# Performance work log

Hardware: AMD Instinct MI355X
Metric: run time of the kernel (lower is better)

## Reference

```python
import jax, jax.numpy as jnp
import numpy as np

BN_EPS = 1e-5  # torch BatchNorm1d default


def setup_inputs() -> dict:
    key = jax.random.key(0)
    k = jax.random.split(key, 5)
    B, D, L = 4096, 4096, 4  # batch, width, num layers (3 hidden + 1 output)
    x = jax.random.normal(k[0], (B, D), dtype=jnp.float32)
    # Per-layer Linear weights stored as [L, in, out]; scaled like xavier-ish init.
    W = jax.random.normal(k[1], (L, D, D), dtype=jnp.float32) * (1.0 / np.sqrt(D))
    b = jax.random.normal(k[2], (L, D), dtype=jnp.float32) * 0.01
    gamma = jax.random.uniform(k[3], (L, D), dtype=jnp.float32, minval=0.5, maxval=1.5)
    beta = jax.random.normal(k[4], (L, D), dtype=jnp.float32) * 0.1
    return {"x": x, "W": W, "b": b, "gamma": gamma, "beta": beta}


def _layer(h, W_l, b_l, gamma_l, beta_l):
    # one big GEMM replaces the per-neuron GEMV loop + stack
    h = h @ W_l + b_l  # [B, out]
    # BatchNorm1d, training mode: biased batch stats over the batch dim
    mu = jnp.mean(h, axis=0)
    var = jnp.var(h, axis=0)
    h = (h - mu) * jax.lax.rsqrt(var + BN_EPS) * gamma_l + beta_l
    return jax.nn.relu(h)


def reference(x, W, b, gamma, beta):
    out = x
    for l in range(W.shape[0]):  # small fixed layer count
        out = _layer(out, W[l], b[l], gamma[l], beta[l])
    # nn.Softmax(dim=0): softmax over the batch dimension, as in the original
    return jax.nn.softmax(out, axis=0)
```

## Files before the change

### kernel.cpp

```cpp
#include <hip/hip_runtime.h>
#include <stdint.h>

#define DIMD 4096
#define DIMB 4096
#define NLAYER 4
#define NT (DIMD / 64)

typedef unsigned short u16;
typedef __attribute__((ext_vector_type(4))) float f32x4;
typedef __attribute__((ext_vector_type(8))) __bf16 bf16x8;

__device__ __forceinline__ u16 f2bf(float f) {
    union { float f; uint32_t u; } v; v.f = f;
    return (u16)((v.u + 0x7fffu + ((v.u >> 16) & 1u)) >> 16);
}

__global__ void k_cvt(const float* __restrict__ in, u16* __restrict__ out) {
    int i = (blockIdx.x * 256 + threadIdx.x) * 4;
    float4 v = *reinterpret_cast<const float4*>(in + i);
    ushort4 r;
    r.x = f2bf(v.x); r.y = f2bf(v.y); r.z = f2bf(v.z); r.w = f2bf(v.w);
    *reinterpret_cast<ushort4*>(out + i) = r;
}

__global__ void k_trans(const float* __restrict__ W, u16* __restrict__ Wt) {
    __shared__ float tile[64][65];
    const int t = threadIdx.x;
    const size_t loff = (size_t)blockIdx.z * DIMD * DIMD;
    const int n0 = blockIdx.x * 64, k0 = blockIdx.y * 64;
    const int kr = t >> 4, c4 = (t & 15) * 4;
    #pragma unroll
    for (int r = 0; r < 4; ++r) {
        float4 v = *reinterpret_cast<const float4*>(W + loff + (size_t)(k0 + kr + r * 16) * DIMD + n0 + c4);
        tile[kr + r * 16][c4 + 0] = v.x;
        tile[kr + r * 16][c4 + 1] = v.y;
        tile[kr + r * 16][c4 + 2] = v.z;
        tile[kr + r * 16][c4 + 3] = v.w;
    }
    __syncthreads();
    const int nr = t >> 4, k4 = (t & 15) * 4;
    #pragma unroll
    for (int r = 0; r < 4; ++r) {
        int n = nr + r * 16;
        ushort4 o;
        o.x = f2bf(tile[k4 + 0][n]);
        o.y = f2bf(tile[k4 + 1][n]);
        o.z = f2bf(tile[k4 + 2][n]);
        o.w = f2bf(tile[k4 + 3][n]);
        *reinterpret_cast<ushort4*>(Wt + loff + (size_t)(n0 + n) * DIMD + k0 + k4) = o;
    }
}

#define GLD(g, l) __builtin_amdgcn_global_load_lds( \
    (__attribute__((address_space(1))) void*)(g),   \
    (__attribute__((address_space(3))) void*)(l), 16, 0, 0)

__global__ __launch_bounds__(512, 2) void k_gemm(
        const u16* __restrict__ A, const u16* __restrict__ Bt,
        const float* __restrict__ bias, float* __restrict__ C,
        float* __restrict__ csum, float* __restrict__ csum2) {
    __shared__ __attribute__((aligned(16))) u16 As[2 * 256 * 64];
    __shared__ __attribute__((aligned(16))) u16 Bs[2 * 256 * 64];
    const int tid = threadIdx.x;
    const int lane = tid & 63, wv = tid >> 6;
    const int wm = wv >> 2, wn = wv & 3;
    const int bm = blockIdx.y, bn = blockIdx.x;
    const int lr = lane & 15, lk = lane >> 4;

    const int r0 = tid >> 3;
    const int cswz = (tid & 7) ^ (r0 & 7);
    const u16* gA = A  + (size_t)(bm * 256 + r0) * DIMD + cswz * 8;
    const u16* gB = Bt + (size_t)(bn * 256 + r0) * DIMD + cswz * 8;

#define STAGE_A(h, t, buf) do { \
    const u16* _s = gA + (size_t)(h) * 128 * DIMD + (size_t)(t) * 64; \
    u16* _d = As + (buf) * 16384 + (h) * 8192 + wv * 512; \
    GLD(_s, _d); GLD(_s + (size_t)64 * DIMD, _d + 4096); \
} while (0)
#define STAGE_B(h, t, buf) do { \
    const u16* _s = gB + (size_t)(h) * 128 * DIMD + (size_t)(t) * 64; \
    u16* _d = Bs + (buf) * 16384 + (h) * 8192 + wv * 512; \
    GLD(_s, _d); GLD(_s + (size_t)64 * DIMD, _d + 4096); \
} while (0)

    int aoff[4][2], boff[2][2];
    #pragma unroll
    for (int mf = 0; mf < 4; ++mf)
        #pragma unroll
        for (int ks = 0; ks < 2; ++ks) {
            int row = wm * 128 + mf * 16 + lr;
            aoff[mf][ks] = row * 64 + ((ks * 4 + lk) ^ (row & 7)) * 8;
        }
    #pragma unroll
    for (int nf = 0; nf < 2; ++nf)
        #pragma unroll
        for (int ks = 0; ks < 2; ++ks) {
            int row = wn * 64 + nf * 16 + lr;
            boff[nf][ks] = row * 64 + ((ks * 4 + lk) ^ (row & 7)) * 8;
        }

    f32x4 acc[8][4] = {};
    bf16x8 al[4][2], ah[4][2], b0[2][2], b1[2][2];

    STAGE_B(0, 0, 0); STAGE_B(1, 0, 0); STAGE_A(0, 0, 0); STAGE_A(1, 0, 0);
    STAGE_B(0, 1, 1); STAGE_B(1, 1, 1); STAGE_A(0, 1, 1); STAGE_A(1, 1, 1);
    asm volatile("s_waitcnt vmcnt(8)" ::: "memory");
    __builtin_amdgcn_s_barrier();

    for (int t = 0; t < NT; ++t) {
        const int cur = t & 1;
        const u16* Ab = As + cur * 16384;
        const u16* Bb = Bs + cur * 16384;
        const bool pf = (t + 2 < NT);

        #pragma unroll
        for (int mf = 0; mf < 4; ++mf)
            #pragma unroll
            for (int ks = 0; ks < 2; ++ks)
                al[mf][ks] = *reinterpret_cast<const bf16x8*>(Ab + aoff[mf][ks]);
        #pragma unroll
        for (int nf = 0; nf < 2; ++nf)
            #pragma unroll
            for (int ks = 0; ks < 2; ++ks)
                b0[nf][ks] = *reinterpret_cast<const bf16x8*>(Bb + boff[nf][ks]);
        #pragma unroll
        for (int nf = 0; nf < 2; ++nf)
            #pragma unroll
            for (int ks = 0; ks < 2; ++ks)
                b1[nf][ks] = *reinterpret_cast<const bf16x8*>(Bb + 2048 + boff[nf][ks]);

        __builtin_amdgcn_s_setprio(1);
        #pragma unroll
        for (int mf = 0; mf < 4; ++mf)
            #pragma unroll
            for (int nf = 0; nf < 2; ++nf)
                #pragma unroll
                for (int ks = 0; ks < 2; ++ks)
                    acc[mf][nf] = __builtin_amdgcn_mfma_f32_16x16x32_bf16(
                        al[mf][ks], b0[nf][ks], acc[mf][nf], 0, 0, 0);
        __builtin_amdgcn_s_setprio(0);

        #pragma unroll
        for (int mf = 0; mf < 4; ++mf)
            #pragma unroll
            for (int ks = 0; ks < 2; ++ks)
                ah[mf][ks] = *reinterpret_cast<const bf16x8*>(Ab + 4096 + aoff[mf][ks]);

        __builtin_amdgcn_s_setprio(1);
        #pragma unroll
        for (int mf = 0; mf < 4; ++mf)
            #pragma unroll
            for (int nf = 0; nf < 2; ++nf)
                #pragma unroll
                for (int ks = 0; ks < 2; ++ks)
                    acc[mf][2 + nf] = __builtin_amdgcn_mfma_f32_16x16x32_bf16(
                        al[mf][ks], b1[nf][ks], acc[mf][2 + nf], 0, 0, 0);
        __builtin_amdgcn_s_setprio(0);

        asm volatile("s_waitcnt lgkmcnt(0)" ::: "memory");
        __builtin_amdgcn_sched_barrier(0);
        __builtin_amdgcn_s_barrier();

        if (pf) {
            STAGE_B(0, t + 2, cur); STAGE_B(1, t + 2, cur);
            STAGE_A(0, t + 2, cur); STAGE_A(1, t + 2, cur);
        }

        __builtin_amdgcn_s_setprio(1);
        #pragma unroll
        for (int mf = 0; mf < 4; ++mf)
            #pragma unroll
            for (int nf = 0; nf < 2; ++nf)
                #pragma unroll
                for (int ks = 0; ks < 2; ++ks)
                    acc[4 + mf][2 + nf] = __builtin_amdgcn_mfma_f32_16x16x32_bf16(
                        ah[mf][ks], b1[nf][ks], acc[4 + mf][2 + nf], 0, 0, 0);
        #pragma unroll
        for (int mf = 0; mf < 4; ++mf)
            #pragma unroll
            for (int nf = 0; nf < 2; ++nf)
                #pragma unroll
                for (int ks = 0; ks < 2; ++ks)
                    acc[4 + mf][nf] = __builtin_amdgcn_mfma_f32_16x16x32_bf16(
                        ah[mf][ks], b0[nf][ks], acc[4 + mf][nf], 0, 0, 0);
        __builtin_amdgcn_s_setprio(0);

        if (pf) asm volatile("s_waitcnt vmcnt(8)" ::: "memory");
        else    asm volatile("s_waitcnt vmcnt(0)" ::: "memory");
        __builtin_amdgcn_s_barrier();
    }

    #pragma unroll
    for (int nh = 0; nh < 2; ++nh)
        #pragma unroll
        for (int nf = 0; nf < 2; ++nf) {
            int n = nh * 2 + nf;
            int col = bn * 256 + wn * 64 + nh * 32 + nf * 16 + lr;
            float bv = bias[col];
            float s1 = 0.f, s2 = 0.f;
            #pragma unroll
            for (int m = 0; m < 8; ++m) {
                int rbase = bm * 256 + wm * 128 + (m >> 2) * 64 + (m & 3) * 16 + lk * 4;
                #pragma unroll
                for (int r = 0; r < 4; ++r) {
                    float v = acc[m][n][r] + bv;
                    C[(size_t)(rbase + r) * DIMD + col] = v;
                    s1 += v; s2 += v * v;
                }
            }
            s1 += __shfl_xor(s1, 16); s1 += __shfl_xor(s1, 32);
            s2 += __shfl_xor(s2, 16); s2 += __shfl_xor(s2, 32);
            if (lk == 0) {
                atomicAdd(&csum[col], s1);
                atomicAdd(&csum2[col], s2);
            }
        }
#undef STAGE_A
#undef STAGE_B
}

__global__ void k_norm(const float* __restrict__ H, const float* __restrict__ sum,
                       const float* __restrict__ sum2, const float* __restrict__ gamma,
                       const float* __restrict__ beta, u16* __restrict__ o) {
    int j = (blockIdx.x * 256 + threadIdx.x) * 4;
    int i0 = blockIdx.y * 128;
    float4 sm = *reinterpret_cast<const float4*>(sum + j);
    float4 s2 = *reinterpret_cast<const float4*>(sum2 + j);
    float4 gm = *reinterpret_cast<const float4*>(gamma + j);
    float4 bt = *reinterpret_cast<const float4*>(beta + j);
    float s[4], tt[4];
    #pragma unroll
    for (int c = 0; c < 4; ++c) {
        float mu = (&sm.x)[c] * (1.0f / DIMB);
        float var = (&s2.x)[c] * (1.0f / DIMB) - mu * mu;
        s[c] = (&gm.x)[c] * rsqrtf(var + 1e-5f);
        tt[c] = (&bt.x)[c] - mu * s[c];
    }
    for (int i = i0; i < i0 + 128; ++i) {
        float4 h = *reinterpret_cast<const float4*>(H + (size_t)i * DIMD + j);
        ushort4 r;
        #pragma unroll
        for (int c = 0; c < 4; ++c)
            (&r.x)[c] = f2bf(fmaxf((&h.x)[c] * s[c] + tt[c], 0.0f));
        *reinterpret_cast<ushort4*>(o + (size_t)i * DIMD + j) = r;
    }
}

__global__ void k_normexp(float* __restrict__ H, const float* __restrict__ sum,
                          const float* __restrict__ sum2, const float* __restrict__ gamma,
                          const float* __restrict__ beta, float* __restrict__ esum) {
    int j = (blockIdx.x * 256 + threadIdx.x) * 4;
    int i0 = blockIdx.y * 128;
    float4 sm = *reinterpret_cast<const float4*>(sum + j);
    float4 s2 = *reinterpret_cast<const float4*>(sum2 + j);
    float4 gm = *reinterpret_cast<const float4*>(gamma + j);
    float4 bt = *reinterpret_cast<const float4*>(beta + j);
    float s[4], tt[4], acc[4] = {0.f, 0.f, 0.f, 0.f};
    #pragma unroll
    for (int c = 0; c < 4; ++c) {
        float mu = (&sm.x)[c] * (1.0f / DIMB);
        float var = (&s2.x)[c] * (1.0f / DIMB) - mu * mu;
        s[c] = (&gm.x)[c] * rsqrtf(var + 1e-5f);
        tt[c] = (&bt.x)[c] - mu * s[c];
    }
    for (int i = i0; i < i0 + 128; ++i) {
        float4 h = *reinterpret_cast<const float4*>(H + (size_t)i * DIMD + j);
        #pragma unroll
        for (int c = 0; c < 4; ++c) {
            float e = __expf(fmaxf((&h.x)[c] * s[c] + tt[c], 0.0f));
            (&h.x)[c] = e;
            acc[c] += e;
        }
        *reinterpret_cast<float4*>(H + (size_t)i * DIMD + j) = h;
    }
    #pragma unroll
    for (int c = 0; c < 4; ++c) atomicAdd(&esum[j + c], acc[c]);
}

__global__ void k_div(float* __restrict__ H, const float* __restrict__ esum) {
    int i = (blockIdx.x * 256 + threadIdx.x) * 4;
    float4 v = *reinterpret_cast<const float4*>(H + i);
    const float4 e = *reinterpret_cast<const float4*>(esum + (i & (DIMD - 1)));
    v.x /= e.x; v.y /= e.y; v.z /= e.z; v.w /= e.w;
    *reinterpret_cast<float4*>(H + i) = v;
}

extern "C" void kernel_launch(void* const* d_in, const int* in_sizes, int n_in,
                              void* d_out, int out_size, void* d_ws, size_t ws_size,
                              hipStream_t stream) {
    (void)in_sizes; (void)n_in; (void)out_size; (void)ws_size;
    const float* x     = (const float*)d_in[0];
    const float* W     = (const float*)d_in[1];
    const float* b     = (const float*)d_in[2];
    const float* gamma = (const float*)d_in[3];
    const float* beta  = (const float*)d_in[4];
    float* out = (float*)d_out;

    char* ws = (char*)d_ws;
    u16*  Abf = (u16*)ws;
    u16*  Wt4 = (u16*)(ws + (size_t)32 * 1024 * 1024);
    float* stats = (float*)(ws + (size_t)160 * 1024 * 1024);
    hipMemsetAsync(stats, 0, (4 * 8192 + 4096) * sizeof(float), stream);

    k_cvt<<<DIMB * DIMD / 1024, 256, 0, stream>>>(x, Abf);
    k_trans<<<dim3(64, 64, 4), 256, 0, stream>>>(W, Wt4);

    for (int l = 0; l < NLAYER; ++l) {
        float* sum = stats + l * 8192;
        float* sum2 = sum + 4096;
        k_gemm<<<dim3(16, 16), 512, 0, stream>>>(Abf, Wt4 + (size_t)l * DIMD * DIMD,
                                                 b + l * DIMD, out, sum, sum2);
        if (l < NLAYER - 1)
            k_norm<<<dim3(4, 32), 256, 0, stream>>>(out, sum, sum2,
                gamma + l * DIMD, beta + l * DIMD, Abf);
        else
            k_normexp<<<dim3(4, 32), 256, 0, stream>>>(out, sum, sum2,
                gamma + l * DIMD, beta + l * DIMD, stats + 32768);
    }
    k_div<<<DIMB * DIMD / 1024, 256, 0, stream>>>(out, stats + 32768);
}
```

Measured before the change: 793.4 us.

## Store GEMM output as bf16, restructure GEMM pipeline, recompute softmax tail

The GEMM epilogue now writes the pre-norm activations as bf16 into a separate buffer instead of fp32, which halves that write and the reads in the norm kernels. The last layer no longer writes exp values and divides in place: it sums exp in one pass, then recomputes exp and normalizes in a final kernel. The GEMM main loop is reordered so A-fragments are loaded in two halves with interleaved barriers, split A/B prefetch, and fewer registers, and workgroup IDs are remapped to improve L2 locality. The norm kernels also launch more, smaller blocks. Rounding the intermediate activations to bf16 adds precision loss before batch norm.

```diff
diff --git a/kernel.cpp b/kernel.cpp
--- a/kernel.cpp
+++ b/kernel.cpp
@@ -13,6 +13,10 @@
 __device__ __forceinline__ u16 f2bf(float f) {
     union { float f; uint32_t u; } v; v.f = f;
     return (u16)((v.u + 0x7fffu + ((v.u >> 16) & 1u)) >> 16);
+}
+__device__ __forceinline__ float bf2f(u16 u) {
+    union { uint32_t u; float f; } v; v.u = ((uint32_t)u) << 16;
+    return v.f;
 }
 
 __global__ void k_cvt(const float* __restrict__ in, u16* __restrict__ out) {
@@ -57,14 +61,16 @@
 
 __global__ __launch_bounds__(512, 2) void k_gemm(
         const u16* __restrict__ A, const u16* __restrict__ Bt,
-        const float* __restrict__ bias, float* __restrict__ C,
+        const float* __restrict__ bias, u16* __restrict__ H,
         float* __restrict__ csum, float* __restrict__ csum2) {
     __shared__ __attribute__((aligned(16))) u16 As[2 * 256 * 64];
     __shared__ __attribute__((aligned(16))) u16 Bs[2 * 256 * 64];
     const int tid = threadIdx.x;
     const int lane = tid & 63, wv = tid >> 6;
     const int wm = wv >> 2, wn = wv & 3;
-    const int bm = blockIdx.y, bn = blockIdx.x;
+    const int bid = blockIdx.y * 16 + blockIdx.x;
+    const int swz = (bid & 7) * 32 + (bid >> 3);
+    const int bm = swz >> 4, bn = swz & 15;
     const int lr = lane & 15, lk = lane >> 4;
 
     const int r0 = tid >> 3;
@@ -100,7 +106,7 @@
         }
 
     f32x4 acc[8][4] = {};
-    bf16x8 al[4][2], ah[4][2], b0[2][2], b1[2][2];
+    bf16x8 a[4][2], b0[2][2], b1[2][2];
 
     STAGE_B(0, 0, 0); STAGE_B(1, 0, 0); STAGE_A(0, 0, 0); STAGE_A(1, 0, 0);
     STAGE_B(0, 1, 1); STAGE_B(1, 1, 1); STAGE_A(0, 1, 1); STAGE_A(1, 1, 1);
@@ -117,35 +123,33 @@
         for (int mf = 0; mf < 4; ++mf)
             #pragma unroll
             for (int ks = 0; ks < 2; ++ks)
-                al[mf][ks] = *reinterpret_cast<const bf16x8*>(Ab + aoff[mf][ks]);
+                a[mf][ks] = *reinterpret_cast<const bf16x8*>(Ab + aoff[mf][ks]);
         #pragma unroll
         for (int nf = 0; nf < 2; ++nf)
             #pragma unroll
             for (int ks = 0; ks < 2; ++ks)
                 b0[nf][ks] = *reinterpret_cast<const bf16x8*>(Bb + boff[nf][ks]);
+        __builtin_amdgcn_s_barrier();
+        asm volatile("s_waitcnt lgkmcnt(0)" ::: "memory");
+        __builtin_amdgcn_s_setprio(1);
+        #pragma unroll
+        for (int mf = 0; mf < 4; ++mf)
+            #pragma unroll
+            for (int nf = 0; nf < 2; ++nf)
+                #pragma unroll
+                for (int ks = 0; ks < 2; ++ks)
+                    acc[mf][nf] = __builtin_amdgcn_mfma_f32_16x16x32_bf16(
+                        a[mf][ks], b0[nf][ks], acc[mf][nf], 0, 0, 0);
+        __builtin_amdgcn_s_setprio(0);
+        __builtin_amdgcn_s_barrier();
+
         #pragma unroll
         for (int nf = 0; nf < 2; ++nf)
             #pragma unroll
             for (int ks = 0; ks < 2; ++ks)
                 b1[nf][ks] = *reinterpret_cast<const bf16x8*>(Bb + 2048 + boff[nf][ks]);
-
-        __builtin_amdgcn_s_setprio(1);
-        #pragma unroll
-        for (int mf = 0; mf < 4; ++mf)
-            #pragma unroll
-            for (int nf = 0; nf < 2; ++nf)
-                #pragma unroll
-                for (int ks = 0; ks < 2; ++ks)
-                    acc[mf][nf] = __builtin_amdgcn_mfma_f32_16x16x32_bf16(
-                        al[mf][ks], b0[nf][ks], acc[mf][nf], 0, 0, 0);
-        __builtin_amdgcn_s_setprio(0);
-
-        #pragma unroll
-        for (int mf = 0; mf < 4; ++mf)
-            #pragma unroll
-            for (int ks = 0; ks < 2; ++ks)
-                ah[mf][ks] = *reinterpret_cast<const bf16x8*>(Ab + 4096 + aoff[mf][ks]);
-
+        __builtin_amdgcn_s_barrier();
+        asm volatile("s_waitcnt lgkmcnt(0)" ::: "memory");
         __builtin_amdgcn_s_setprio(1);
         #pragma unroll
         for (int mf = 0; mf < 4; ++mf)
@@ -154,18 +158,18 @@
                 #pragma unroll
                 for (int ks = 0; ks < 2; ++ks)
                     acc[mf][2 + nf] = __builtin_amdgcn_mfma_f32_16x16x32_bf16(
-                        al[mf][ks], b1[nf][ks], acc[mf][2 + nf], 0, 0, 0);
+                        a[mf][ks], b1[nf][ks], acc[mf][2 + nf], 0, 0, 0);
         __builtin_amdgcn_s_setprio(0);
-
+        __builtin_amdgcn_s_barrier();
+
+        #pragma unroll
+        for (int mf = 0; mf < 4; ++mf)
+            #pragma unroll
+            for (int ks = 0; ks < 2; ++ks)
+                a[mf][ks] = *reinterpret_cast<const bf16x8*>(Ab + 4096 + aoff[mf][ks]);
+        if (pf) { STAGE_B(0, t + 2, cur); STAGE_B(1, t + 2, cur); }
+        __builtin_amdgcn_s_barrier();
         asm volatile("s_waitcnt lgkmcnt(0)" ::: "memory");
-        __builtin_amdgcn_sched_barrier(0);
-        __builtin_amdgcn_s_barrier();
-
-        if (pf) {
-            STAGE_B(0, t + 2, cur); STAGE_B(1, t + 2, cur);
-            STAGE_A(0, t + 2, cur); STAGE_A(1, t + 2, cur);
-        }
-
         __builtin_amdgcn_s_setprio(1);
         #pragma unroll
         for (int mf = 0; mf < 4; ++mf)
@@ -174,7 +178,12 @@
                 #pragma unroll
                 for (int ks = 0; ks < 2; ++ks)
                     acc[4 + mf][2 + nf] = __builtin_amdgcn_mfma_f32_16x16x32_bf16(
-                        ah[mf][ks], b1[nf][ks], acc[4 + mf][2 + nf], 0, 0, 0);
+                        a[mf][ks], b1[nf][ks], acc[4 + mf][2 + nf], 0, 0, 0);
+        __builtin_amdgcn_s_setprio(0);
+        __builtin_amdgcn_s_barrier();
+
+        if (pf) { STAGE_A(0, t + 2, cur); STAGE_A(1, t + 2, cur); }
+        __builtin_amdgcn_s_setprio(1);
         #pragma unroll
         for (int mf = 0; mf < 4; ++mf)
             #pragma unroll
@@ -182,9 +191,8 @@
                 #pragma unroll
                 for (int ks = 0; ks < 2; ++ks)
                     acc[4 + mf][nf] = __builtin_amdgcn_mfma_f32_16x16x32_bf16(
-                        ah[mf][ks], b0[nf][ks], acc[4 + mf][nf], 0, 0, 0);
+                        a[mf][ks], b0[nf][ks], acc[4 + mf][nf], 0, 0, 0);
         __builtin_amdgcn_s_setprio(0);
-
         if (pf) asm volatile("s_waitcnt vmcnt(8)" ::: "memory");
         else    asm volatile("s_waitcnt vmcnt(0)" ::: "memory");
         __builtin_amdgcn_s_barrier();
@@ -204,7 +212,7 @@
                 #pragma unroll
                 for (int r = 0; r < 4; ++r) {
                     float v = acc[m][n][r] + bv;
-                    C[(size_t)(rbase + r) * DIMD + col] = v;
+                    H[(size_t)(rbase + r) * DIMD + col] = f2bf(v);
                     s1 += v; s2 += v * v;
                 }
             }
@@ -219,11 +227,11 @@
 #undef STAGE_B
 }
 
-__global__ void k_norm(const float* __restrict__ H, const float* __restrict__ sum,
+__global__ void k_norm(const u16* __restrict__ H, const float* __restrict__ sum,
                        const float* __restrict__ sum2, const float* __restrict__ gamma,
                        const float* __restrict__ beta, u16* __restrict__ o) {
     int j = (blockIdx.x * 256 + threadIdx.x) * 4;
-    int i0 = blockIdx.y * 128;
+    int i0 = blockIdx.y * 32;
     float4 sm = *reinterpret_cast<const float4*>(sum + j);
     float4 s2 = *reinterpret_cast<const float4*>(sum2 + j);
     float4 gm = *reinterpret_cast<const float4*>(gamma + j);
@@ -236,21 +244,21 @@
         s[c] = (&gm.x)[c] * rsqrtf(var + 1e-5f);
         tt[c] = (&bt.x)[c] - mu * s[c];
     }
-    for (int i = i0; i < i0 + 128; ++i) {
-        float4 h = *reinterpret_cast<const float4*>(H + (size_t)i * DIMD + j);
+    for (int i = i0; i < i0 + 32; ++i) {
+        ushort4 h = *reinterpret_cast<const ushort4*>(H + (size_t)i * DIMD + j);
         ushort4 r;
         #pragma unroll
         for (int c = 0; c < 4; ++c)
-            (&r.x)[c] = f2bf(fmaxf((&h.x)[c] * s[c] + tt[c], 0.0f));
+            (&r.x)[c] = f2bf(fmaxf(bf2f((&h.x)[c]) * s[c] + tt[c], 0.0f));
         *reinterpret_cast<ushort4*>(o + (size_t)i * DIMD + j) = r;
     }
 }
 
-__global__ void k_normexp(float* __restrict__ H, const float* __restrict__ sum,
-                          const float* __restrict__ sum2, const float* __restrict__ gamma,
-                          const float* __restrict__ beta, float* __restrict__ esum) {
+__global__ void k_esum(const u16* __restrict__ H, const float* __restrict__ sum,
+                       const float* __restrict__ sum2, const float* __restrict__ gamma,
+                       const float* __restrict__ beta, float* __restrict__ esum) {
     int j = (blockIdx.x * 256 + threadIdx.x) * 4;
-    int i0 = blockIdx.y * 128;
+    int i0 = blockIdx.y * 32;
     float4 sm = *reinterpret_cast<const float4*>(sum + j);
     float4 s2 = *reinterpret_cast<const float4*>(sum2 + j);
     float4 gm = *reinterpret_cast<const float4*>(gamma + j);
@@ -263,26 +271,44 @@
         s[c] = (&gm.x)[c] * rsqrtf(var + 1e-5f);
         tt[c] = (&bt.x)[c] - mu * s[c];
     }
-    for (int i = i0; i < i0 + 128; ++i) {
-        float4 h = *reinterpret_cast<const float4*>(H + (size_t)i * DIMD + j);
-        #pragma unroll
-        for (int c = 0; c < 4; ++c) {
-            float e = __expf(fmaxf((&h.x)[c] * s[c] + tt[c], 0.0f));
-            (&h.x)[c] = e;
-            acc[c] += e;
-        }
-        *reinterpret_cast<float4*>(H + (size_t)i * DIMD + j) = h;
+    for (int i = i0; i < i0 + 32; ++i) {
+        ushort4 h = *reinterpret_cast<const ushort4*>(H + (size_t)i * DIMD + j);
+        #pragma unroll
+        for (int c = 0; c < 4; ++c)
+            acc[c] += __expf(fmaxf(bf2f((&h.x)[c]) * s[c] + tt[c], 0.0f));
     }
     #pragma unroll
     for (int c = 0; c < 4; ++c) atomicAdd(&esum[j + c], acc[c]);
 }
 
-__global__ void k_div(float* __restrict__ H, const float* __restrict__ esum) {
-    int i = (blockIdx.x * 256 + threadIdx.x) * 4;
-    float4 v = *reinterpret_cast<const float4*>(H + i);
-    const float4 e = *reinterpret_cast<const float4*>(esum + (i & (DIMD - 1)));
-    v.x /= e.x; v.y /= e.y; v.z /= e.z; v.w /= e.w;
-    *reinterpret_cast<float4*>(H + i) = v;
+__global__ void k_final(const u16* __restrict__ H, const float* __restrict__ sum,
+                        const float* __restrict__ sum2, const float* __restrict__ gamma,
+                        const float* __restrict__ beta, const float* __restrict__ esum,
+                        float* __restrict__ out) {
+    int j = (blockIdx.x * 256 + threadIdx.x) * 4;
+    int i0 = blockIdx.y * 32;
+    float4 sm = *reinterpret_cast<const float4*>(sum + j);
+    float4 s2 = *reinterpret_cast<const float4*>(sum2 + j);
+    float4 gm = *reinterpret_cast<const float4*>(gamma + j);
+    float4 bt = *reinterpret_cast<const float4*>(beta + j);
+    float4 es = *reinterpret_cast<const float4*>(esum + j);
+    float s[4], tt[4], inv[4];
+    #pragma unroll
+    for (int c = 0; c < 4; ++c) {
+        float mu = (&sm.x)[c] * (1.0f / DIMB);
+        float var = (&s2.x)[c] * (1.0f / DIMB) - mu * mu;
+        s[c] = (&gm.x)[c] * rsqrtf(var + 1e-5f);
+        tt[c] = (&bt.x)[c] - mu * s[c];
+        inv[c] = 1.0f / (&es.x)[c];
+    }
+    for (int i = i0; i < i0 + 32; ++i) {
+        ushort4 h = *reinterpret_cast<const ushort4*>(H + (size_t)i * DIMD + j);
+        float4 o;
+        #pragma unroll
+        for (int c = 0; c < 4; ++c)
+            (&o.x)[c] = __expf(fmaxf(bf2f((&h.x)[c]) * s[c] + tt[c], 0.0f)) * inv[c];
+        *reinterpret_cast<float4*>(out + (size_t)i * DIMD + j) = o;
+    }
 }
 
 extern "C" void kernel_launch(void* const* d_in, const int* in_sizes, int n_in,
@@ -299,7 +325,8 @@
     char* ws = (char*)d_ws;
     u16*  Abf = (u16*)ws;
     u16*  Wt4 = (u16*)(ws + (size_t)32 * 1024 * 1024);
-    float* stats = (float*)(ws + (size_t)160 * 1024 * 1024);
+    u16*  Hbf = (u16*)(ws + (size_t)160 * 1024 * 1024);
+    float* stats = (float*)(ws + (size_t)192 * 1024 * 1024);
     hipMemsetAsync(stats, 0, (4 * 8192 + 4096) * sizeof(float), stream);
 
     k_cvt<<<DIMB * DIMD / 1024, 256, 0, stream>>>(x, Abf);
@@ -309,13 +336,14 @@
         float* sum = stats + l * 8192;
         float* sum2 = sum + 4096;
         k_gemm<<<dim3(16, 16), 512, 0, stream>>>(Abf, Wt4 + (size_t)l * DIMD * DIMD,
-                                                 b + l * DIMD, out, sum, sum2);
+                                                 b + l * DIMD, Hbf, sum, sum2);
         if (l < NLAYER - 1)
-            k_norm<<<dim3(4, 32), 256, 0, stream>>>(out, sum, sum2,
+            k_norm<<<dim3(4, 128), 256, 0, stream>>>(Hbf, sum, sum2,
                 gamma + l * DIMD, beta + l * DIMD, Abf);
         else
-            k_normexp<<<dim3(4, 32), 256, 0, stream>>>(out, sum, sum2,
+            k_esum<<<dim3(4, 128), 256, 0, stream>>>(Hbf, sum, sum2,
                 gamma + l * DIMD, beta + l * DIMD, stats + 32768);
     }
-    k_div<<<DIMB * DIMD / 1024, 256, 0, stream>>>(out, stats + 32768);
-}
+    k_final<<<dim3(4, 128), 256, 0, stream>>>(Hbf, stats + 3 * 8192, stats + 3 * 8192 + 4096,
+        gamma + 3 * DIMD, beta + 3 * DIMD, stats + 32768, out);
+}
```

Result: faster. 731.1 us (-7.9%).
